# Performance work log

Hardware: AMD Instinct MI355X
Metric: run time of the kernel (lower is better)

Reference implementation:

```python
import jax, jax.numpy as jnp
import numpy as np

LEVEL = 8
THRESHOLD = 0.1
INV_SQRT2 = 0.7071067811865476  # 1/sqrt(2), db1 (Haar) filter coefficient

# Static frequency-order permutation: pywt get_level(order='freq') places the
# natural-order (path-lex: aa,ad,da,dd,...) node n at frequency position gray(n).
_g = np.arange(2 ** LEVEL)
_FREQ_PERM = np.argsort(_g ^ (_g >> 1))  # freq[j] = natural[_FREQ_PERM[j]]


def setup_inputs() -> dict:
    key = jax.random.key(0)
    x = jax.random.normal(key, (128, 65536), dtype=jnp.float32)
    return {"x": x}


def _wavelet_packet_leaves(x):
    """Full db1 wavelet-packet tree to LEVEL; returns [B, 2^L, T/2^L] in freq order.

    For Haar with even-length inputs, pywt's symmetric extension is a no-op:
    a[k] = (x[2k]+x[2k+1])/sqrt2, d[k] = (x[2k]-x[2k+1])/sqrt2.
    """
    B, T = x.shape
    c = x[:, None, :]  # [B, nodes=1, len=T]
    for _ in range(LEVEL):
        ev = c[..., 0::2]
        od = c[..., 1::2]
        a = (ev + od) * INV_SQRT2
        d = (ev - od) * INV_SQRT2
        # interleave children (a,d) adjacent -> natural (path-lex) node order
        c = jnp.concatenate([a[:, :, None, :], d[:, :, None, :]], axis=2)
        c = c.reshape(B, -1, a.shape[-1])
    return c[:, _FREQ_PERM, :]


def reference(x):
    coeffs = _wavelet_packet_leaves(x)          # [B, 2^L, n]
    p = coeffs * coeffs
    p = p / (jnp.sum(p, axis=-1, keepdims=True) + 1e-8)
    entropy = -jnp.sum(p * jnp.log(p + 1e-8), axis=-1)  # [B, 2^L]
    keep = entropy > THRESHOLD                           # [B, 2^L] bool
    # Original returns per-batch stacks of kept nodes (variable length);
    # jit-friendly equivalent: zero out pruned nodes and return the mask.
    out = jnp.where(keep[..., None], coeffs, jnp.zeros((), coeffs.dtype))
    return out, entropy, keep
```

## Files before the change

kernel.cpp:

```cpp
#include <hip/hip_runtime.h>

static constexpr int BROWS = 128;
static constexpr int T     = 65536;
static constexpr int CL    = 256;
static constexpr int NCH   = 256;
static constexpr int NODES = 256;
static constexpr int KG    = 32;
static constexpr int LSTR  = 257;

__device__ __forceinline__ int freq_pos(int h) {
    unsigned r = __brev((unsigned)h) >> 24;
    return (int)(r ^ (r >> 1));
}

__device__ __forceinline__ void bfly01(float4& v) {
    float4 w;
    w.x = v.x + v.y; w.y = v.x - v.y;
    w.z = v.z + v.w; w.w = v.z - v.w;
    v.x = w.x + w.z; v.z = w.x - w.z;
    v.y = w.y + w.w; v.w = w.y - w.w;
}

template<int CTRL>
__device__ __forceinline__ float xchg_dpp(float v) {
    return __builtin_bit_cast(float,
        __builtin_amdgcn_update_dpp(0, __builtin_bit_cast(int, v), CTRL, 0xF, 0xF, true));
}

template<int CTRL>
__device__ __forceinline__ void stage_dpp(float4& v1, float4& v2, float sgn) {
    float o;
    o = xchg_dpp<CTRL>(v1.x); v1.x = fmaf(sgn, v1.x, o);
    o = xchg_dpp<CTRL>(v1.y); v1.y = fmaf(sgn, v1.y, o);
    o = xchg_dpp<CTRL>(v1.z); v1.z = fmaf(sgn, v1.z, o);
    o = xchg_dpp<CTRL>(v1.w); v1.w = fmaf(sgn, v1.w, o);
    o = xchg_dpp<CTRL>(v2.x); v2.x = fmaf(sgn, v2.x, o);
    o = xchg_dpp<CTRL>(v2.y); v2.y = fmaf(sgn, v2.y, o);
    o = xchg_dpp<CTRL>(v2.z); v2.z = fmaf(sgn, v2.z, o);
    o = xchg_dpp<CTRL>(v2.w); v2.w = fmaf(sgn, v2.w, o);
}

__device__ __forceinline__ void stage_shfl(float4& v1, float4& v2, float sgn, int mask) {
    float o;
    o = __shfl_xor(v1.x, mask, 64); v1.x = fmaf(sgn, v1.x, o);
    o = __shfl_xor(v1.y, mask, 64); v1.y = fmaf(sgn, v1.y, o);
    o = __shfl_xor(v1.z, mask, 64); v1.z = fmaf(sgn, v1.z, o);
    o = __shfl_xor(v1.w, mask, 64); v1.w = fmaf(sgn, v1.w, o);
    o = __shfl_xor(v2.x, mask, 64); v2.x = fmaf(sgn, v2.x, o);
    o = __shfl_xor(v2.y, mask, 64); v2.y = fmaf(sgn, v2.y, o);
    o = __shfl_xor(v2.z, mask, 64); v2.z = fmaf(sgn, v2.z, o);
    o = __shfl_xor(v2.w, mask, 64); v2.w = fmaf(sgn, v2.w, o);
}

__global__ __launch_bounds__(256) void wht_kernel(const float* __restrict__ x,
                                                  float* __restrict__ coeffs,
                                                  float* __restrict__ part) {
    __shared__ float lds[KG][LSTR];

    const int b    = blockIdx.x >> 3;
    const int kg   = blockIdx.x & 7;
    const int k0   = kg * KG;
    const int lane = threadIdx.x & 63;
    const int wave = threadIdx.x >> 6;
    const int half = lane >> 5;
    const int L    = lane & 31;

    const float* xb = x + (size_t)b * T;

    int npos1[4], npos2[4];
    #pragma unroll
    for (int i = 0; i < 4; ++i) {
        npos1[i] = freq_pos(4 * L + i);
        npos2[i] = freq_pos(128 + 4 * L + i);
    }
    float A1[4] = {0.f,0.f,0.f,0.f}, B1[4] = {0.f,0.f,0.f,0.f};
    float A2[4] = {0.f,0.f,0.f,0.f}, B2[4] = {0.f,0.f,0.f,0.f};

    const float sgn0 = 1.0f - 2.0f * (float)((L >> 0) & 1);
    const float sgn1 = 1.0f - 2.0f * (float)((L >> 1) & 1);
    const float sgn2 = 1.0f - 2.0f * (float)((L >> 2) & 1);
    const float sgn3 = 1.0f - 2.0f * (float)((L >> 3) & 1);
    const float sgn4 = 1.0f - 2.0f * (float)((L >> 4) & 1);

    #pragma unroll
    for (int it = 0; it < 4; ++it) {
        const int kl = wave * 8 + it * 2 + half;
        const float* cp = xb + (size_t)(k0 + kl) * CL + 4 * L;
        float4 v1 = *(const float4*)(cp);
        float4 v2 = *(const float4*)(cp + 128);

        float4 t;
        t.x = v1.x - v2.x; t.y = v1.y - v2.y; t.z = v1.z - v2.z; t.w = v1.w - v2.w;
        v1.x += v2.x; v1.y += v2.y; v1.z += v2.z; v1.w += v2.w;
        v2 = t;

        bfly01(v1);
        bfly01(v2);

        stage_dpp<0xB1>(v1, v2, sgn0);
        stage_dpp<0x4E>(v1, v2, sgn1);
        stage_shfl(v1, v2, sgn2, 4);
        stage_dpp<0x128>(v1, v2, sgn3);
        stage_shfl(v1, v2, sgn4, 16);

        float c1[4] = {v1.x*0.0625f, v1.y*0.0625f, v1.z*0.0625f, v1.w*0.0625f};
        float c2[4] = {v2.x*0.0625f, v2.y*0.0625f, v2.z*0.0625f, v2.w*0.0625f};
        #pragma unroll
        for (int i = 0; i < 4; ++i) {
            const float s1 = c1[i] * c1[i];
            A1[i] += s1;
            B1[i] += s1 * __logf(s1 + 1e-35f);
            lds[kl][npos1[i]] = c1[i];
            const float s2 = c2[i] * c2[i];
            A2[i] += s2;
            B2[i] += s2 * __logf(s2 + 1e-35f);
            lds[kl][npos2[i]] = c2[i];
        }
    }
    __syncthreads();

    float* ob = coeffs + (size_t)b * T + k0;
    const int kk = (threadIdx.x & 7) * 4;
    const int m0 = threadIdx.x >> 3;
    #pragma unroll
    for (int p = 0; p < 8; ++p) {
        const int m = p * 32 + m0;
        float4 v;
        v.x = lds[kk + 0][m];
        v.y = lds[kk + 1][m];
        v.z = lds[kk + 2][m];
        v.w = lds[kk + 3][m];
        *(float4*)(ob + (size_t)m * NCH + kk) = v;
    }
    __syncthreads();

    #pragma unroll
    for (int i = 0; i < 4; ++i) {
        A1[i] += __shfl_xor(A1[i], 32, 64); B1[i] += __shfl_xor(B1[i], 32, 64);
        A2[i] += __shfl_xor(A2[i], 32, 64); B2[i] += __shfl_xor(B2[i], 32, 64);
    }
    float* pl = &lds[0][0];
    if (half == 0) {
        #pragma unroll
        for (int i = 0; i < 4; ++i) {
            pl[wave * 512 + npos1[i]]       = A1[i];
            pl[wave * 512 + 256 + npos1[i]] = B1[i];
            pl[wave * 512 + npos2[i]]       = A2[i];
            pl[wave * 512 + 256 + npos2[i]] = B2[i];
        }
    }
    __syncthreads();

    const int n = threadIdx.x;
    const float A = pl[n] + pl[512 + n] + pl[1024 + n] + pl[1536 + n];
    const float B = pl[256 + n] + pl[768 + n] + pl[1280 + n] + pl[1792 + n];
    float* pp = part + (size_t)blockIdx.x * 512;
    pp[n]       = A;
    pp[256 + n] = B;
}

__global__ __launch_bounds__(256) void finalize_kernel(const float* __restrict__ part,
                                                       float* __restrict__ coeffs,
                                                       float* __restrict__ entropy,
                                                       float* __restrict__ keep) {
    const int row = blockIdx.x * 256 + threadIdx.x;
    const int b = row >> 8;
    const int n = row & 255;

    float A = 0.f, B = 0.f;
    #pragma unroll
    for (int g = 0; g < 8; ++g) {
        const float* p = part + (size_t)(b * 8 + g) * 512;
        A += p[n];
        B += p[256 + n];
    }

    const float S = A + 1e-8f;
    const float e = (A * __logf(S) - B) / S;
    const bool kp = e > 0.1f;

    entropy[row] = e;
    keep[row]    = kp ? 1.0f : 0.0f;

    if (!kp) {
        float4 z = make_float4(0.f, 0.f, 0.f, 0.f);
        float4* cp = (float4*)(coeffs + (size_t)row * NCH);
        #pragma unroll
        for (int j = 0; j < NCH / 4; ++j) cp[j] = z;
    }
}

extern "C" void kernel_launch(void* const* d_in, const int* in_sizes, int n_in,
                              void* d_out, int out_size, void* d_ws, size_t ws_size,
                              hipStream_t stream) {
    const float* x = (const float*)d_in[0];

    float* coeffs  = (float*)d_out;
    float* entropy = coeffs + (size_t)BROWS * NODES * NCH;
    float* keepf   = entropy + (size_t)BROWS * NODES;

    float* part = (float*)d_ws;

    wht_kernel<<<dim3(BROWS * (NCH / KG)), dim3(256), 0, stream>>>(x, coeffs, part);
    finalize_kernel<<<dim3(BROWS * NODES / 256), dim3(256), 0, stream>>>(part, coeffs, entropy, keepf);
}
```

Before: 84.38 us.

## Fuse finalize into WHT kernel via last-block atomic counter per row

```diff
diff --git a/kernel.cpp b/kernel.cpp
--- a/kernel.cpp
+++ b/kernel.cpp
@@ -52,10 +52,14 @@
     o = __shfl_xor(v2.w, mask, 64); v2.w = fmaf(sgn, v2.w, o);
 }
 
-__global__ __launch_bounds__(256) void wht_kernel(const float* __restrict__ x,
-                                                  float* __restrict__ coeffs,
-                                                  float* __restrict__ part) {
+__global__ __launch_bounds__(256) void wht_fused(const float* __restrict__ x,
+                                                 float* __restrict__ coeffs,
+                                                 float* __restrict__ part,
+                                                 int* __restrict__ cnt,
+                                                 float* __restrict__ entropy,
+                                                 float* __restrict__ keep) {
     __shared__ float lds[KG][LSTR];
+    __shared__ int s_last;
 
     const int b    = blockIdx.x >> 3;
     const int kg   = blockIdx.x & 7;
@@ -157,36 +161,35 @@
     float* pp = part + (size_t)blockIdx.x * 512;
     pp[n]       = A;
     pp[256 + n] = B;
-}
-
-__global__ __launch_bounds__(256) void finalize_kernel(const float* __restrict__ part,
-                                                       float* __restrict__ coeffs,
-                                                       float* __restrict__ entropy,
-                                                       float* __restrict__ keep) {
-    const int row = blockIdx.x * 256 + threadIdx.x;
-    const int b = row >> 8;
-    const int n = row & 255;
-
-    float A = 0.f, B = 0.f;
+
+    __threadfence();
+    __syncthreads();
+    if (threadIdx.x == 0)
+        s_last = (atomicAdd(&cnt[b], 1) == 7) ? 1 : 0;
+    __syncthreads();
+    if (!s_last) return;
+    __threadfence();
+
+    const int nn = threadIdx.x;
+    float Af = 0.f, Bf = 0.f;
+    const float* pb = part + (size_t)b * 8 * 512;
     #pragma unroll
     for (int g = 0; g < 8; ++g) {
-        const float* p = part + (size_t)(b * 8 + g) * 512;
-        A += p[n];
-        B += p[256 + n];
-    }
-
-    const float S = A + 1e-8f;
-    const float e = (A * __logf(S) - B) / S;
+        Af += pb[g * 512 + nn];
+        Bf += pb[g * 512 + 256 + nn];
+    }
+    const float S = Af + 1e-8f;
+    const float e = (Af * __logf(S) - Bf) / S;
     const bool kp = e > 0.1f;
 
-    entropy[row] = e;
-    keep[row]    = kp ? 1.0f : 0.0f;
+    entropy[b * NODES + nn] = e;
+    keep[b * NODES + nn]    = kp ? 1.0f : 0.0f;
 
     if (!kp) {
         float4 z = make_float4(0.f, 0.f, 0.f, 0.f);
-        float4* cp = (float4*)(coeffs + (size_t)row * NCH);
+        float4* cp4 = (float4*)(coeffs + ((size_t)b * NODES + nn) * NCH);
         #pragma unroll
-        for (int j = 0; j < NCH / 4; ++j) cp[j] = z;
+        for (int j = 0; j < NCH / 4; ++j) cp4[j] = z;
     }
 }
 
@@ -200,7 +203,10 @@
     float* keepf   = entropy + (size_t)BROWS * NODES;
 
     float* part = (float*)d_ws;
-
-    wht_kernel<<<dim3(BROWS * (NCH / KG)), dim3(256), 0, stream>>>(x, coeffs, part);
-    finalize_kernel<<<dim3(BROWS * NODES / 256), dim3(256), 0, stream>>>(part, coeffs, entropy, keepf);
-}
+    int*   cnt  = (int*)((char*)d_ws + (size_t)2 * 1024 * 1024);
+
+    hipMemsetAsync(cnt, 0, BROWS * sizeof(int), stream);
+
+    wht_fused<<<dim3(BROWS * (NCH / KG)), dim3(256), 0, stream>>>(
+        x, coeffs, part, cnt, entropy, keepf);
+}
```

Result: slower. 231.3 us (+174.1%).

## Fuse transform and finalize into one per-row kernel with prefetch

Applied to the files above, without the earlier changes.

```diff
diff --git a/kernel.cpp b/kernel.cpp
--- a/kernel.cpp
+++ b/kernel.cpp
@@ -6,7 +6,9 @@
 static constexpr int NCH   = 256;
 static constexpr int NODES = 256;
 static constexpr int KG    = 32;
+static constexpr int NPH   = NCH / KG;
 static constexpr int LSTR  = 257;
+static constexpr int NTHR  = 512;
 
 __device__ __forceinline__ int freq_pos(int h) {
     unsigned r = __brev((unsigned)h) >> 24;
@@ -52,14 +54,13 @@
     o = __shfl_xor(v2.w, mask, 64); v2.w = fmaf(sgn, v2.w, o);
 }
 
-__global__ __launch_bounds__(256) void wht_kernel(const float* __restrict__ x,
-                                                  float* __restrict__ coeffs,
-                                                  float* __restrict__ part) {
+__global__ __launch_bounds__(NTHR) void wht_row(const float* __restrict__ x,
+                                                float* __restrict__ coeffs,
+                                                float* __restrict__ entropy,
+                                                float* __restrict__ keep) {
     __shared__ float lds[KG][LSTR];
 
-    const int b    = blockIdx.x >> 3;
-    const int kg   = blockIdx.x & 7;
-    const int k0   = kg * KG;
+    const int b    = blockIdx.x;
     const int lane = threadIdx.x & 63;
     const int wave = threadIdx.x >> 6;
     const int half = lane >> 5;
@@ -82,57 +83,80 @@
     const float sgn3 = 1.0f - 2.0f * (float)((L >> 3) & 1);
     const float sgn4 = 1.0f - 2.0f * (float)((L >> 4) & 1);
 
-    #pragma unroll
-    for (int it = 0; it < 4; ++it) {
-        const int kl = wave * 8 + it * 2 + half;
-        const float* cp = xb + (size_t)(k0 + kl) * CL + 4 * L;
-        float4 v1 = *(const float4*)(cp);
-        float4 v2 = *(const float4*)(cp + 128);
-
-        float4 t;
-        t.x = v1.x - v2.x; t.y = v1.y - v2.y; t.z = v1.z - v2.z; t.w = v1.w - v2.w;
-        v1.x += v2.x; v1.y += v2.y; v1.z += v2.z; v1.w += v2.w;
-        v2 = t;
-
-        bfly01(v1);
-        bfly01(v2);
-
-        stage_dpp<0xB1>(v1, v2, sgn0);
-        stage_dpp<0x4E>(v1, v2, sgn1);
-        stage_shfl(v1, v2, sgn2, 4);
-        stage_dpp<0x128>(v1, v2, sgn3);
-        stage_shfl(v1, v2, sgn4, 16);
-
-        float c1[4] = {v1.x*0.0625f, v1.y*0.0625f, v1.z*0.0625f, v1.w*0.0625f};
-        float c2[4] = {v2.x*0.0625f, v2.y*0.0625f, v2.z*0.0625f, v2.w*0.0625f};
+    const int kl0 = wave * 4 + half;
+    const int kl1 = wave * 4 + 2 + half;
+    const int col = 4 * L;
+
+    float4 c0a = *(const float4*)(xb + (size_t)kl0 * CL + col);
+    float4 c0b = *(const float4*)(xb + (size_t)kl0 * CL + col + 128);
+    float4 c1a = *(const float4*)(xb + (size_t)kl1 * CL + col);
+    float4 c1b = *(const float4*)(xb + (size_t)kl1 * CL + col + 128);
+
+    #pragma unroll
+    for (int ph = 0; ph < NPH; ++ph) {
+        float4 n0a, n0b, n1a, n1b;
+        if (ph + 1 < NPH) {
+            const float* q0 = xb + (size_t)((ph + 1) * KG + kl0) * CL + col;
+            const float* q1 = xb + (size_t)((ph + 1) * KG + kl1) * CL + col;
+            n0a = *(const float4*)(q0);
+            n0b = *(const float4*)(q0 + 128);
+            n1a = *(const float4*)(q1);
+            n1b = *(const float4*)(q1 + 128);
+        }
+
         #pragma unroll
-        for (int i = 0; i < 4; ++i) {
-            const float s1 = c1[i] * c1[i];
-            A1[i] += s1;
-            B1[i] += s1 * __logf(s1 + 1e-35f);
-            lds[kl][npos1[i]] = c1[i];
-            const float s2 = c2[i] * c2[i];
-            A2[i] += s2;
-            B2[i] += s2 * __logf(s2 + 1e-35f);
-            lds[kl][npos2[i]] = c2[i];
-        }
-    }
-    __syncthreads();
-
-    float* ob = coeffs + (size_t)b * T + k0;
-    const int kk = (threadIdx.x & 7) * 4;
-    const int m0 = threadIdx.x >> 3;
-    #pragma unroll
-    for (int p = 0; p < 8; ++p) {
-        const int m = p * 32 + m0;
-        float4 v;
-        v.x = lds[kk + 0][m];
-        v.y = lds[kk + 1][m];
-        v.z = lds[kk + 2][m];
-        v.w = lds[kk + 3][m];
-        *(float4*)(ob + (size_t)m * NCH + kk) = v;
-    }
-    __syncthreads();
+        for (int it = 0; it < 2; ++it) {
+            const int kl = (it == 0) ? kl0 : kl1;
+            float4 v1 = (it == 0) ? c0a : c1a;
+            float4 v2 = (it == 0) ? c0b : c1b;
+
+            float4 t;
+            t.x = v1.x - v2.x; t.y = v1.y - v2.y; t.z = v1.z - v2.z; t.w = v1.w - v2.w;
+            v1.x += v2.x; v1.y += v2.y; v1.z += v2.z; v1.w += v2.w;
+            v2 = t;
+
+            bfly01(v1);
+            bfly01(v2);
+
+            stage_dpp<0xB1>(v1, v2, sgn0);
+            stage_dpp<0x4E>(v1, v2, sgn1);
+            stage_shfl(v1, v2, sgn2, 4);
+            stage_dpp<0x128>(v1, v2, sgn3);
+            stage_shfl(v1, v2, sgn4, 16);
+
+            float c1r[4] = {v1.x*0.0625f, v1.y*0.0625f, v1.z*0.0625f, v1.w*0.0625f};
+            float c2r[4] = {v2.x*0.0625f, v2.y*0.0625f, v2.z*0.0625f, v2.w*0.0625f};
+            #pragma unroll
+            for (int i = 0; i < 4; ++i) {
+                const float s1 = c1r[i] * c1r[i];
+                A1[i] += s1;
+                B1[i] += s1 * __logf(s1 + 1e-35f);
+                lds[kl][npos1[i]] = c1r[i];
+                const float s2 = c2r[i] * c2r[i];
+                A2[i] += s2;
+                B2[i] += s2 * __logf(s2 + 1e-35f);
+                lds[kl][npos2[i]] = c2r[i];
+            }
+        }
+        __syncthreads();
+
+        float* ob = coeffs + (size_t)b * T + ph * KG;
+        const int kk = (threadIdx.x & 7) * 4;
+        const int m0 = threadIdx.x >> 3;
+        #pragma unroll
+        for (int p = 0; p < 4; ++p) {
+            const int m = p * 64 + m0;
+            float4 v;
+            v.x = lds[kk + 0][m];
+            v.y = lds[kk + 1][m];
+            v.z = lds[kk + 2][m];
+            v.w = lds[kk + 3][m];
+            *(float4*)(ob + (size_t)m * NCH + kk) = v;
+        }
+        __syncthreads();
+
+        c0a = n0a; c0b = n0b; c1a = n1a; c1b = n1b;
+    }
 
     #pragma unroll
     for (int i = 0; i < 4; ++i) {
@@ -151,42 +175,28 @@
     }
     __syncthreads();
 
-    const int n = threadIdx.x;
-    const float A = pl[n] + pl[512 + n] + pl[1024 + n] + pl[1536 + n];
-    const float B = pl[256 + n] + pl[768 + n] + pl[1280 + n] + pl[1792 + n];
-    float* pp = part + (size_t)blockIdx.x * 512;
-    pp[n]       = A;
-    pp[256 + n] = B;
-}
-
-__global__ __launch_bounds__(256) void finalize_kernel(const float* __restrict__ part,
-                                                       float* __restrict__ coeffs,
-                                                       float* __restrict__ entropy,
-                                                       float* __restrict__ keep) {
-    const int row = blockIdx.x * 256 + threadIdx.x;
-    const int b = row >> 8;
-    const int n = row & 255;
-
-    float A = 0.f, B = 0.f;
-    #pragma unroll
-    for (int g = 0; g < 8; ++g) {
-        const float* p = part + (size_t)(b * 8 + g) * 512;
-        A += p[n];
-        B += p[256 + n];
-    }
-
-    const float S = A + 1e-8f;
-    const float e = (A * __logf(S) - B) / S;
-    const bool kp = e > 0.1f;
-
-    entropy[row] = e;
-    keep[row]    = kp ? 1.0f : 0.0f;
-
-    if (!kp) {
-        float4 z = make_float4(0.f, 0.f, 0.f, 0.f);
-        float4* cp = (float4*)(coeffs + (size_t)row * NCH);
-        #pragma unroll
-        for (int j = 0; j < NCH / 4; ++j) cp[j] = z;
+    const int idx = threadIdx.x;
+    float s = 0.f;
+    #pragma unroll
+    for (int w = 0; w < 8; ++w) s += pl[w * 512 + idx];
+    pl[idx] = s;
+    __syncthreads();
+
+    if (idx < NODES) {
+        const float A = pl[idx];
+        const float B = pl[256 + idx];
+        const float S = A + 1e-8f;
+        const float e = (A * __logf(S) - B) / S;
+        const bool kp = e > 0.1f;
+
+        entropy[b * NODES + idx] = e;
+        keep[b * NODES + idx]    = kp ? 1.0f : 0.0f;
+
+        if (!kp) {
+            float4 z = make_float4(0.f, 0.f, 0.f, 0.f);
+            float4* cp = (float4*)(coeffs + ((size_t)b * NODES + idx) * NCH);
+            for (int j = 0; j < NCH / 4; ++j) cp[j] = z;
+        }
     }
 }
 
@@ -199,8 +209,7 @@
     float* entropy = coeffs + (size_t)BROWS * NODES * NCH;
     float* keepf   = entropy + (size_t)BROWS * NODES;
 
-    float* part = (float*)d_ws;
-
-    wht_kernel<<<dim3(BROWS * (NCH / KG)), dim3(256), 0, stream>>>(x, coeffs, part);
-    finalize_kernel<<<dim3(BROWS * NODES / 256), dim3(256), 0, stream>>>(part, coeffs, entropy, keepf);
-}
+    (void)d_ws; (void)ws_size;
+
+    wht_row<<<dim3(BROWS), dim3(NTHR), 0, stream>>>(x, coeffs, entropy, keepf);
+}
```

Result: slower. 91.17 us (+8.0%).
